# Optimization experiments

Measured on AMD Instinct MI355X. Metric: run time of the kernel, lower is better.

Reference implementation:

```python
import jax, jax.numpy as jnp
import numpy as np

B, L, D = 16, 1024, 256  # batch, c_len == q_len (required by the expand/add in the source), 2*d_model


def mask_logits(x, m):
    # Faithful to the source's (unusual) masking: x*m + x*(1-m)*1e30
    return x * m + x * (1.0 - m) * 1e30


def setup_inputs() -> dict:
    key = jax.random.key(0)
    k = jax.random.split(key, 7)
    c = jax.random.normal(k[0], (B, L, D), dtype=jnp.float32)
    q = jax.random.normal(k[1], (B, L, D), dtype=jnp.float32)
    c_mask = jnp.ones((B, 1, L), dtype=jnp.float32)
    q_mask = jnp.ones((B, 1, L), dtype=jnp.float32)
    # Learned parameters (nn.Parameter zeros in the source; random here so the test is non-degenerate)
    c_weight = jax.random.normal(k[2], (D, 1), dtype=jnp.float32) * 0.05
    q_weight = jax.random.normal(k[3], (D, 1), dtype=jnp.float32) * 0.05
    cq_weight = jax.random.normal(k[4], (1, 1, D), dtype=jnp.float32) * 0.05
    bias = jnp.zeros((1,), dtype=jnp.float32)
    return {"c": c, "q": q, "c_mask": c_mask, "q_mask": q_mask,
            "c_weight": c_weight, "q_weight": q_weight,
            "cq_weight": cq_weight, "bias": bias}


def reference(c, q, c_mask, q_mask, c_weight, q_weight, cq_weight, bias):
    # Dropout treated as identity (inference) for a deterministic reference.
    s0 = jnp.matmul(c, c_weight)                      # [B, L, 1] -> broadcasts over q_len
    s1 = jnp.swapaxes(jnp.matmul(c, q_weight), 1, 2)  # [B, 1, L] (source uses c here, not q)
    s2 = jnp.einsum('bid,bjd->bij', c * cq_weight, q) # [B, L, L]
    S = s0 + s1 + s2 + bias                           # trilinear similarity
    S1 = jax.nn.softmax(mask_logits(S, q_mask), axis=-1)              # [B, Lc, Lq]
    C2Q = jnp.matmul(S1, q)                                           # [B, Lc, D]
    # torch F.softmax with no dim on a 3D tensor defaults to dim=0 (legacy behavior) -> axis=0
    S2 = jax.nn.softmax(mask_logits(jnp.swapaxes(S, 1, 2), c_mask), axis=0)  # [B, Lq, Lc]
    S2 = jnp.matmul(S1, S2)                                           # [B, Lc, Lc]
    Q2C = jnp.matmul(S2, c)                                           # [B, Lc, D]
    # torch.cat default dim=0 -> [4B, Lc, D]
    return jnp.concatenate((c, C2Q, c * C2Q, c * Q2C), axis=0)
```

## Files before the change

### kernel.cpp

```cpp
#include <hip/hip_runtime.h>

typedef __bf16 bf16;
typedef _Float16 f16;
typedef __attribute__((ext_vector_type(8))) __bf16 bf16x8;
typedef __attribute__((ext_vector_type(4))) __bf16 bf16x4;
typedef __attribute__((ext_vector_type(8))) _Float16 f16x8;
typedef __attribute__((ext_vector_type(4))) _Float16 f16x4;
typedef __attribute__((ext_vector_type(4))) float f32x4;

constexpr int Bn = 16, Ln = 1024, Dn = 256;

__device__ __forceinline__ float maskf(float m) { return m + (1.0f - m) * 1e30f; }

__device__ __forceinline__ void gload16(const void* g, void* l) {
  __builtin_amdgcn_global_load_lds((const __attribute__((address_space(1))) void*)g,
                                   (__attribute__((address_space(3))) void*)l, 16, 0, 0);
}

__device__ __forceinline__ void stageA64(const bf16* __restrict__ A, int lda, int k0,
                                         bf16* lA, int tid, int wid) {
  int row = tid >> 2, kk = (tid & 3) << 3;
  gload16(A + (size_t)row * lda + k0 + kk, lA + (wid << 6) * 8);
}
__device__ __forceinline__ void stageB128(const bf16* __restrict__ B, int ldb, int k0,
                                          bf16* lB, int tid, int wid) {
#pragma unroll
  for (int p = 0; p < 2; ++p) {
    int c0 = tid + (p << 8);
    int row = c0 >> 2, kk = (c0 & 3) << 3;
    gload16(B + (size_t)row * ldb + k0 + kk, lB + ((p << 8) + (wid << 6)) * 8);
  }
}

__global__ __launch_bounds__(256) void k_prep2(
    const float* __restrict__ c, const float* __restrict__ q,
    const float* __restrict__ cw, const float* __restrict__ qw,
    const float* __restrict__ cqw, bf16* __restrict__ cm, bf16* __restrict__ qb,
    bf16* __restrict__ cT, bf16* __restrict__ qT,
    float* __restrict__ s0, float* __restrict__ s1, float* __restrict__ outc) {
  __shared__ __align__(16) bf16 tc[32][264];
  __shared__ __align__(16) bf16 tq[32][264];
  int blk = blockIdx.x;
  int b = blk >> 5;
  int l0 = (blk & 31) << 5;
  int t = threadIdx.x;
  int rl = t >> 3;
  int c0 = (t & 7) << 5;
  int grow = b * Ln + l0 + rl;
  size_t base = (size_t)grow * Dn + c0;
  float4 cv[8], qv[8];
#pragma unroll
  for (int k = 0; k < 8; ++k) {
    cv[k] = *(const float4*)&c[base + k * 4];
    qv[k] = *(const float4*)&q[base + k * 4];
  }
  float d0 = 0.f, d1 = 0.f;
#pragma unroll
  for (int k = 0; k < 8; ++k) {
    float4 w = *(const float4*)&cw[c0 + k * 4];
    float4 u = *(const float4*)&qw[c0 + k * 4];
    d0 += cv[k].x * w.x + cv[k].y * w.y + cv[k].z * w.z + cv[k].w * w.w;
    d1 += cv[k].x * u.x + cv[k].y * u.y + cv[k].z * u.z + cv[k].w * u.w;
  }
  d0 += __shfl_xor(d0, 1); d0 += __shfl_xor(d0, 2); d0 += __shfl_xor(d0, 4);
  d1 += __shfl_xor(d1, 1); d1 += __shfl_xor(d1, 2); d1 += __shfl_xor(d1, 4);
  if ((t & 7) == 0) { s0[grow] = d0; s1[grow] = d1; }
#pragma unroll
  for (int k = 0; k < 8; ++k) *(float4*)&outc[base + k * 4] = cv[k];
#pragma unroll
  for (int k2 = 0; k2 < 4; ++k2) {
    float4 m0 = *(const float4*)&cqw[c0 + k2 * 8];
    float4 m1 = *(const float4*)&cqw[c0 + k2 * 8 + 4];
    bf16x8 vm, vq, vc;
#pragma unroll
    for (int e = 0; e < 8; ++e) {
      float cvv = ((const float*)&cv[k2 * 2 + (e >> 2)])[e & 3];
      float qvv = ((const float*)&qv[k2 * 2 + (e >> 2)])[e & 3];
      float mw = (e < 4) ? ((const float*)&m0)[e] : ((const float*)&m1)[e - 4];
      vm[e] = (bf16)(cvv * mw);
      vq[e] = (bf16)qvv;
      vc[e] = (bf16)cvv;
    }
    *(bf16x8*)&cm[base + k2 * 8] = vm;
    *(bf16x8*)&qb[base + k2 * 8] = vq;
    *(bf16x8*)&tc[rl][c0 + k2 * 8] = vc;
    *(bf16x8*)&tq[rl][c0 + k2 * 8] = vq;
  }
  __syncthreads();
  int d = t;
  size_t tb = ((size_t)b * Dn + d) * Ln + l0;
  bf16x8 o[4];
#pragma unroll
  for (int j = 0; j < 4; ++j)
#pragma unroll
    for (int e = 0; e < 8; ++e) o[j][e] = tc[j * 8 + e][d];
#pragma unroll
  for (int j = 0; j < 4; ++j) *(bf16x8*)&cT[tb + j * 8] = o[j];
#pragma unroll
  for (int j = 0; j < 4; ++j)
#pragma unroll
    for (int e = 0; e < 8; ++e) o[j][e] = tq[j * 8 + e][d];
#pragma unroll
  for (int j = 0; j < 4; ++j) *(bf16x8*)&qT[tb + j * 8] = o[j];
}

__global__ __launch_bounds__(256) void g_s(const bf16* __restrict__ Am,
                                           const bf16* __restrict__ Bm,
                                           const float* __restrict__ s0,
                                           const float* __restrict__ s1,
                                           const float* __restrict__ bias,
                                           f16* __restrict__ S) {
  __shared__ __align__(16) bf16 lds[2][256 * 32];
  int f = blockIdx.x;
  int o = (f & 7) * 128 + (f >> 3);
  int bx = o & 7, by = (o >> 3) & 7, b = o >> 6;
  const bf16* Ab = Am + (size_t)b * Ln * Dn + (size_t)by * 128 * Dn;
  const bf16* Bb = Bm + (size_t)b * Ln * Dn + (size_t)bx * 128 * Dn;
  const int tid = threadIdx.x, wid = tid >> 6, lane = tid & 63;
  const int r = lane & 15, h = lane >> 4, wr = wid >> 1, wc = wid & 1;
  f32x4 acc[4][4];
  f32x4 zero = {0.f, 0.f, 0.f, 0.f};
#pragma unroll
  for (int i = 0; i < 4; ++i)
#pragma unroll
    for (int j = 0; j < 4; ++j) acc[i][j] = zero;

  stageB128(Ab, Dn, 0, &lds[0][0], tid, wid);
  stageB128(Bb, Dn, 0, &lds[0][128 * 32], tid, wid);
  __syncthreads();
  for (int t = 0; t < 8; ++t) {
    int cur = t & 1;
    if (t < 7) {
      stageB128(Ab, Dn, (t + 1) * 32, &lds[cur ^ 1][0], tid, wid);
      stageB128(Bb, Dn, (t + 1) * 32, &lds[cur ^ 1][128 * 32], tid, wid);
    }
    const bf16* lA = &lds[cur][0];
    const bf16* lB = &lds[cur][128 * 32];
    bf16x8 av[4], bv[4];
#pragma unroll
    for (int i = 0; i < 4; ++i) {
      av[i] = *(const bf16x8*)(lA + ((wr << 6) + (i << 4) + r) * 32 + (h << 3));
      bv[i] = *(const bf16x8*)(lB + ((wc << 6) + (i << 4) + r) * 32 + (h << 3));
    }
#pragma unroll
    for (int i = 0; i < 4; ++i)
#pragma unroll
      for (int j = 0; j < 4; ++j)
        acc[i][j] = __builtin_amdgcn_mfma_f32_16x16x32_bf16(av[i], bv[j], acc[i][j], 0, 0, 0);
    __syncthreads();
  }
  int grow = by * 128 + wr * 64, gcol = bx * 128 + wc * 64;
  float bvv = bias[0];
  size_t sb = (size_t)b * Ln * Ln;
#pragma unroll
  for (int j = 0; j < 4; ++j) {
    int n = gcol + j * 16 + r;
    float v1 = s1[b * Ln + n];
#pragma unroll
    for (int i = 0; i < 4; ++i) {
      int mb = grow + i * 16 + h * 4;
#pragma unroll
      for (int g = 0; g < 4; ++g) {
        float v0 = s0[b * Ln + mb + g];
        S[sb + (size_t)(mb + g) * Ln + n] = (f16)(acc[i][j][g] + v0 + v1 + bvv);
      }
    }
  }
}

__global__ __launch_bounds__(256) void k_rowsoftmax(const f16* __restrict__ S,
                                                    const float* __restrict__ qmask,
                                                    bf16* __restrict__ P1) {
  int t = threadIdx.x;
  int row = blockIdx.x * 4 + (t >> 6);
  int b = row >> 10;
  int lane = t & 63;
  const f16* Sr = S + (size_t)row * Ln;
  const float* qm = qmask + (size_t)b * Ln;
  float v[16];
  float mx = -3.4e38f;
#pragma unroll
  for (int p = 0; p < 2; ++p) {
    f16x8 x = ((const f16x8*)Sr)[lane + (p << 6)];
    float4 m0 = ((const float4*)qm)[(lane + (p << 6)) * 2];
    float4 m1 = ((const float4*)qm)[(lane + (p << 6)) * 2 + 1];
    float mm[8] = {m0.x, m0.y, m0.z, m0.w, m1.x, m1.y, m1.z, m1.w};
#pragma unroll
    for (int e = 0; e < 8; ++e) {
      float xv = (float)x[e] * maskf(mm[e]);
      v[8 * p + e] = xv;
      mx = fmaxf(mx, xv);
    }
  }
#pragma unroll
  for (int off = 32; off; off >>= 1) mx = fmaxf(mx, __shfl_xor(mx, off));
  float sum = 0.f;
#pragma unroll
  for (int k = 0; k < 16; ++k) {
    v[k] = __expf(v[k] - mx);
    sum += v[k];
  }
#pragma unroll
  for (int off = 32; off; off >>= 1) sum += __shfl_xor(sum, off);
  float inv = 1.0f / sum;
  bf16* Pr = P1 + (size_t)row * Ln;
#pragma unroll
  for (int p = 0; p < 2; ++p) {
    bf16x8 o;
#pragma unroll
    for (int e = 0; e < 8; ++e) o[e] = (bf16)(v[8 * p + e] * inv);
    ((bf16x8*)Pr)[lane + (p << 6)] = o;
  }
}

__global__ __launch_bounds__(256) void k_bp2(const f16* __restrict__ S,
                                             const float* __restrict__ cmask,
                                             bf16* __restrict__ P2) {
  __shared__ __align__(16) bf16 tile[16][32][36];
  int i0 = blockIdx.y * 32, j0 = blockIdx.x * 32;
  int t = threadIdx.x;
  int ti = t >> 3, tj4 = (t & 7) << 2;
  int i = i0 + ti;
  const f16* Sp = S + (size_t)i * Ln + j0 + tj4;
  float fm[16];
#pragma unroll
  for (int b = 0; b < 16; ++b) fm[b] = maskf(cmask[b * Ln + i]);
  float m[4] = {-3.4e38f, -3.4e38f, -3.4e38f, -3.4e38f};
#pragma unroll
  for (int b = 0; b < 16; ++b) {
    f16x4 u = *(const f16x4*)(Sp + (size_t)b * Ln * Ln);
#pragma unroll
    for (int g = 0; g < 4; ++g) m[g] = fmaxf(m[g], (float)u[g] * fm[b]);
  }
  float s[4] = {0.f, 0.f, 0.f, 0.f};
#pragma unroll
  for (int b = 0; b < 16; ++b) {
    f16x4 u = *(const f16x4*)(Sp + (size_t)b * Ln * Ln);
#pragma unroll
    for (int g = 0; g < 4; ++g) s[g] += __expf((float)u[g] * fm[b] - m[g]);
  }
#pragma unroll
  for (int g = 0; g < 4; ++g) s[g] = 1.0f / s[g];
#pragma unroll
  for (int b = 0; b < 16; ++b) {
    f16x4 u = *(const f16x4*)(Sp + (size_t)b * Ln * Ln);
#pragma unroll
    for (int g = 0; g < 4; ++g)
      tile[b][tj4 + g][ti] = (bf16)(__expf((float)u[g] * fm[b] - m[g]) * s[g]);
  }
  __syncthreads();
  int jl = t >> 3, i4 = (t & 7) << 2;
#pragma unroll
  for (int b = 0; b < 16; ++b) {
    *(bf16x4*)&P2[((size_t)b * Ln + j0 + jl) * Ln + i0 + i4] =
        *(const bf16x4*)&tile[b][jl][i4];
  }
}

__global__ __launch_bounds__(256) void g_t(const bf16* __restrict__ cT,
                                           const bf16* __restrict__ P2,
                                           bf16* __restrict__ TT) {
  __shared__ __align__(16) bf16 lds[2][192 * 32];
  int f = blockIdx.x;
  int o = (f & 7) * 64 + (f >> 3);
  int b = o >> 5, md = (o >> 3) & 3, nb = o & 7;
  const bf16* Ab = cT + (size_t)b * Dn * Ln + (size_t)md * 64 * Ln;
  const bf16* Bb = P2 + (size_t)b * Ln * Ln + (size_t)nb * 128 * Ln;
  const int tid = threadIdx.x, wid = tid >> 6, lane = tid & 63;
  const int r = lane & 15, h = lane >> 4, wr = wid >> 1, wc = wid & 1;
  f32x4 acc[2][4];
  f32x4 zero = {0.f, 0.f, 0.f, 0.f};
#pragma unroll
  for (int i = 0; i < 2; ++i)
#pragma unroll
    for (int j = 0; j < 4; ++j) acc[i][j] = zero;

  stageA64(Ab, Ln, 0, &lds[0][0], tid, wid);
  stageB128(Bb, Ln, 0, &lds[0][64 * 32], tid, wid);
  __syncthreads();
  for (int t = 0; t < 32; ++t) {
    int cur = t & 1;
    if (t < 31) {
      stageA64(Ab, Ln, (t + 1) * 32, &lds[cur ^ 1][0], tid, wid);
      stageB128(Bb, Ln, (t + 1) * 32, &lds[cur ^ 1][64 * 32], tid, wid);
    }
    const bf16* lA = &lds[cur][0];
    const bf16* lB = &lds[cur][64 * 32];
    bf16x8 av[2], bv[4];
#pragma unroll
    for (int i = 0; i < 2; ++i)
      av[i] = *(const bf16x8*)(lA + ((wr << 5) + (i << 4) + r) * 32 + (h << 3));
#pragma unroll
    for (int j = 0; j < 4; ++j)
      bv[j] = *(const bf16x8*)(lB + ((wc << 6) + (j << 4) + r) * 32 + (h << 3));
#pragma unroll
    for (int i = 0; i < 2; ++i)
#pragma unroll
      for (int j = 0; j < 4; ++j)
        acc[i][j] = __builtin_amdgcn_mfma_f32_16x16x32_bf16(av[i], bv[j], acc[i][j], 0, 0, 0);
    __syncthreads();
  }
  size_t ob = (size_t)b * Dn * Ln;
  int dbase = md * 64 + wr * 32, cbase = nb * 128 + wc * 64;
#pragma unroll
  for (int i = 0; i < 2; ++i)
#pragma unroll
    for (int j = 0; j < 4; ++j) {
      int n = cbase + j * 16 + r;
#pragma unroll
      for (int g = 0; g < 4; ++g)
        TT[ob + (size_t)(dbase + i * 16 + h * 4 + g) * Ln + n] = (bf16)acc[i][j][g];
    }
}

__global__ __launch_bounds__(256) void g_cq(const bf16* __restrict__ P1,
                                            const bf16* __restrict__ qT,
                                            const bf16* __restrict__ TT,
                                            const float* __restrict__ c,
                                            float* __restrict__ out) {
  __shared__ __align__(16) bf16 lds[2][192 * 32];
  int f = blockIdx.x;
  int o = (f & 7) * 128 + (f >> 3);
  int b = o >> 6, by = (o >> 2) & 15, bx = o & 3;
  const bf16* Ab = P1 + (size_t)b * Ln * Ln + (size_t)by * 64 * Ln;
  const bf16* B1 = qT + (size_t)b * Dn * Ln + (size_t)bx * 64 * Ln;
  const bf16* B2 = TT + (size_t)b * Dn * Ln + (size_t)bx * 64 * Ln;
  const int tid = threadIdx.x, wid = tid >> 6, lane = tid & 63;
  const int r = lane & 15, h = lane >> 4, wr = wid >> 1, wc = wid & 1;
  f32x4 acc1[2][2], acc2[2][2];
  f32x4 zero = {0.f, 0.f, 0.f, 0.f};
#pragma unroll
  for (int i = 0; i < 2; ++i)
#pragma unroll
    for (int j = 0; j < 2; ++j) { acc1[i][j] = zero; acc2[i][j] = zero; }

  stageA64(Ab, Ln, 0, &lds[0][0], tid, wid);
  stageA64(B1, Ln, 0, &lds[0][2048], tid, wid);
  stageA64(B2, Ln, 0, &lds[0][4096], tid, wid);
  __syncthreads();
  for (int t = 0; t < 32; ++t) {
    int cur = t & 1;
    if (t < 31) {
      stageA64(Ab, Ln, (t + 1) * 32, &lds[cur ^ 1][0], tid, wid);
      stageA64(B1, Ln, (t + 1) * 32, &lds[cur ^ 1][2048], tid, wid);
      stageA64(B2, Ln, (t + 1) * 32, &lds[cur ^ 1][4096], tid, wid);
    }
    const bf16* lA = &lds[cur][0];
    const bf16* lB1 = &lds[cur][2048];
    const bf16* lB2 = &lds[cur][4096];
    bf16x8 av[2], bv[2];
#pragma unroll
    for (int i = 0; i < 2; ++i)
      av[i] = *(const bf16x8*)(lA + ((wr << 5) + (i << 4) + r) * 32 + (h << 3));
#pragma unroll
    for (int j = 0; j < 2; ++j)
      bv[j] = *(const bf16x8*)(lB1 + ((wc << 5) + (j << 4) + r) * 32 + (h << 3));
#pragma unroll
    for (int i = 0; i < 2; ++i)
#pragma unroll
      for (int j = 0; j < 2; ++j)
        acc1[i][j] = __builtin_amdgcn_mfma_f32_16x16x32_bf16(av[i], bv[j], acc1[i][j], 0, 0, 0);
#pragma unroll
    for (int j = 0; j < 2; ++j)
      bv[j] = *(const bf16x8*)(lB2 + ((wc << 5) + (j << 4) + r) * 32 + (h << 3));
#pragma unroll
    for (int i = 0; i < 2; ++i)
#pragma unroll
      for (int j = 0; j < 2; ++j)
        acc2[i][j] = __builtin_amdgcn_mfma_f32_16x16x32_bf16(av[i], bv[j], acc2[i][j], 0, 0, 0);
    __syncthreads();
  }

  int grow = by * 64 + wr * 32, gcol = bx * 64 + wc * 32;
  const float* cb = c + (size_t)b * Ln * Dn;
  float* o1 = out + (size_t)(1 * Bn + b) * Ln * Dn;
  float* o2 = out + (size_t)(2 * Bn + b) * Ln * Dn;
  float* o3 = out + (size_t)(3 * Bn + b) * Ln * Dn;
#pragma unroll
  for (int j = 0; j < 2; ++j) {
    int n = gcol + j * 16 + r;
#pragma unroll
    for (int i = 0; i < 2; ++i) {
      int mb = grow + i * 16 + h * 4;
#pragma unroll
      for (int g = 0; g < 4; ++g) {
        float v1 = acc1[i][j][g];
        float v2 = acc2[i][j][g];
        size_t off = (size_t)(mb + g) * Dn + n;
        float cc = cb[off];
        o1[off] = v1;
        o2[off] = cc * v1;
        o3[off] = cc * v2;
      }
    }
  }
}

extern "C" void kernel_launch(void* const* d_in, const int* in_sizes, int n_in,
                              void* d_out, int out_size, void* d_ws, size_t ws_size,
                              hipStream_t stream) {
  const float* c = (const float*)d_in[0];
  const float* q = (const float*)d_in[1];
  const float* cmask = (const float*)d_in[2];
  const float* qmask = (const float*)d_in[3];
  const float* cw = (const float*)d_in[4];
  const float* qw = (const float*)d_in[5];
  const float* cqw = (const float*)d_in[6];
  const float* bias = (const float*)d_in[7];
  float* out = (float*)d_out;

  char* w = (char*)d_ws;
  f16* S = (f16*)w;       w += (size_t)Bn * Ln * Ln * 2;
  bf16* P1 = (bf16*)w;    w += (size_t)Bn * Ln * Ln * 2;
  bf16* P2 = (bf16*)w;    w += (size_t)Bn * Ln * Ln * 2;
  bf16* cm = (bf16*)w;    w += (size_t)Bn * Ln * Dn * 2;
  bf16* qb = (bf16*)w;    w += (size_t)Bn * Ln * Dn * 2;
  bf16* cT = (bf16*)w;    w += (size_t)Bn * Dn * Ln * 2;
  bf16* qT = (bf16*)w;    w += (size_t)Bn * Dn * Ln * 2;
  bf16* TT = (bf16*)w;    w += (size_t)Bn * Dn * Ln * 2;
  float* s0 = (float*)w;  w += (size_t)Bn * Ln * 4;
  float* s1 = (float*)w;  w += (size_t)Bn * Ln * 4;
  if ((size_t)(w - (char*)d_ws) > ws_size) return;

  k_prep2<<<dim3(Bn * Ln / 32), 256, 0, stream>>>(c, q, cw, qw, cqw, cm, qb, cT, qT, s0, s1, out);
  g_s<<<dim3(1024), 256, 0, stream>>>(cm, qb, s0, s1, bias, S);
  k_rowsoftmax<<<dim3(Bn * Ln / 4), 256, 0, stream>>>(S, qmask, P1);
  k_bp2<<<dim3(Ln / 32, Ln / 32), 256, 0, stream>>>(S, cmask, P2);
  g_t<<<dim3(512), 256, 0, stream>>>(cT, P2, TT);
  g_cq<<<dim3(1024), 256, 0, stream>>>(P1, qT, TT, c, out);
}
```

Before: 132.4 us.

## Double K-tile depth to 64 with XOR-swizzled LDS layout in g_t and g_cq

The two GEMM kernels g_t and g_cq now stage 64-wide K slices instead of 32. That halves the main-loop iterations and the block-wide barriers, and each stage holds two MFMA k-steps. The LDS tiles use a 64-element row stride with an XOR swizzle of the 16-byte slot by row, meant to avoid bank conflicts on the fragment reads. LDS use per block doubles, to 48KB in g_t, which may lower occupancy.

```diff
diff --git a/kernel.cpp b/kernel.cpp
--- a/kernel.cpp
+++ b/kernel.cpp
@@ -17,11 +17,6 @@
                                    (__attribute__((address_space(3))) void*)l, 16, 0, 0);
 }
 
-__device__ __forceinline__ void stageA64(const bf16* __restrict__ A, int lda, int k0,
-                                         bf16* lA, int tid, int wid) {
-  int row = tid >> 2, kk = (tid & 3) << 3;
-  gload16(A + (size_t)row * lda + k0 + kk, lA + (wid << 6) * 8);
-}
 __device__ __forceinline__ void stageB128(const bf16* __restrict__ B, int ldb, int k0,
                                           bf16* lB, int tid, int wid) {
 #pragma unroll
@@ -30,6 +25,31 @@
     int row = c0 >> 2, kk = (c0 & 3) << 3;
     gload16(B + (size_t)row * ldb + k0 + kk, lB + ((p << 8) + (wid << 6)) * 8);
   }
+}
+
+__device__ __forceinline__ void stageSwz64(const bf16* __restrict__ G, int ldg, int k0,
+                                           bf16* L, int tid, int wid) {
+#pragma unroll
+  for (int p = 0; p < 2; ++p) {
+    int u = tid + (p << 8);
+    int row = u >> 3, s = u & 7;
+    int kk = ((s ^ (row & 7)) << 3);
+    gload16(G + (size_t)row * ldg + k0 + kk, L + ((p << 8) + (wid << 6)) * 8);
+  }
+}
+__device__ __forceinline__ void stageSwz128(const bf16* __restrict__ G, int ldg, int k0,
+                                            bf16* L, int tid, int wid) {
+#pragma unroll
+  for (int p = 0; p < 4; ++p) {
+    int u = tid + (p << 8);
+    int row = u >> 3, s = u & 7;
+    int kk = ((s ^ (row & 7)) << 3);
+    gload16(G + (size_t)row * ldg + k0 + kk, L + ((p << 8) + (wid << 6)) * 8);
+  }
+}
+
+__device__ __forceinline__ const bf16* swzp(const bf16* L, int row, int slot) {
+  return L + row * 64 + ((slot ^ (row & 7)) << 3);
 }
 
 __global__ __launch_bounds__(256) void k_prep2(
@@ -260,7 +280,7 @@
 __global__ __launch_bounds__(256) void g_t(const bf16* __restrict__ cT,
                                            const bf16* __restrict__ P2,
                                            bf16* __restrict__ TT) {
-  __shared__ __align__(16) bf16 lds[2][192 * 32];
+  __shared__ __align__(16) bf16 lds[2][192 * 64];
   int f = blockIdx.x;
   int o = (f & 7) * 64 + (f >> 3);
   int b = o >> 5, md = (o >> 3) & 3, nb = o & 7;
@@ -275,29 +295,33 @@
 #pragma unroll
     for (int j = 0; j < 4; ++j) acc[i][j] = zero;
 
-  stageA64(Ab, Ln, 0, &lds[0][0], tid, wid);
-  stageB128(Bb, Ln, 0, &lds[0][64 * 32], tid, wid);
+  stageSwz64(Ab, Ln, 0, &lds[0][0], tid, wid);
+  stageSwz128(Bb, Ln, 0, &lds[0][64 * 64], tid, wid);
   __syncthreads();
-  for (int t = 0; t < 32; ++t) {
+  for (int t = 0; t < 16; ++t) {
     int cur = t & 1;
-    if (t < 31) {
-      stageA64(Ab, Ln, (t + 1) * 32, &lds[cur ^ 1][0], tid, wid);
-      stageB128(Bb, Ln, (t + 1) * 32, &lds[cur ^ 1][64 * 32], tid, wid);
+    if (t < 15) {
+      stageSwz64(Ab, Ln, (t + 1) * 64, &lds[cur ^ 1][0], tid, wid);
+      stageSwz128(Bb, Ln, (t + 1) * 64, &lds[cur ^ 1][64 * 64], tid, wid);
     }
     const bf16* lA = &lds[cur][0];
-    const bf16* lB = &lds[cur][64 * 32];
-    bf16x8 av[2], bv[4];
-#pragma unroll
-    for (int i = 0; i < 2; ++i)
-      av[i] = *(const bf16x8*)(lA + ((wr << 5) + (i << 4) + r) * 32 + (h << 3));
-#pragma unroll
-    for (int j = 0; j < 4; ++j)
-      bv[j] = *(const bf16x8*)(lB + ((wc << 6) + (j << 4) + r) * 32 + (h << 3));
-#pragma unroll
-    for (int i = 0; i < 2; ++i)
+    const bf16* lB = &lds[cur][64 * 64];
+#pragma unroll
+    for (int kk2 = 0; kk2 < 2; ++kk2) {
+      int slot = (kk2 << 2) | h;
+      bf16x8 av[2], bv[4];
+#pragma unroll
+      for (int i = 0; i < 2; ++i)
+        av[i] = *(const bf16x8*)swzp(lA, (wr << 5) + (i << 4) + r, slot);
 #pragma unroll
       for (int j = 0; j < 4; ++j)
-        acc[i][j] = __builtin_amdgcn_mfma_f32_16x16x32_bf16(av[i], bv[j], acc[i][j], 0, 0, 0);
+        bv[j] = *(const bf16x8*)swzp(lB, (wc << 6) + (j << 4) + r, slot);
+#pragma unroll
+      for (int i = 0; i < 2; ++i)
+#pragma unroll
+        for (int j = 0; j < 4; ++j)
+          acc[i][j] = __builtin_amdgcn_mfma_f32_16x16x32_bf16(av[i], bv[j], acc[i][j], 0, 0, 0);
+    }
     __syncthreads();
   }
   size_t ob = (size_t)b * Dn * Ln;
@@ -318,7 +342,7 @@
                                             const bf16* __restrict__ TT,
                                             const float* __restrict__ c,
                                             float* __restrict__ out) {
-  __shared__ __align__(16) bf16 lds[2][192 * 32];
+  __shared__ __align__(16) bf16 lds[2][192 * 64];
   int f = blockIdx.x;
   int o = (f & 7) * 128 + (f >> 3);
   int b = o >> 6, by = (o >> 2) & 15, bx = o & 3;
@@ -334,40 +358,44 @@
 #pragma unroll
     for (int j = 0; j < 2; ++j) { acc1[i][j] = zero; acc2[i][j] = zero; }
 
-  stageA64(Ab, Ln, 0, &lds[0][0], tid, wid);
-  stageA64(B1, Ln, 0, &lds[0][2048], tid, wid);
-  stageA64(B2, Ln, 0, &lds[0][4096], tid, wid);
+  stageSwz64(Ab, Ln, 0, &lds[0][0], tid, wid);
+  stageSwz64(B1, Ln, 0, &lds[0][4096], tid, wid);
+  stageSwz64(B2, Ln, 0, &lds[0][8192], tid, wid);
   __syncthreads();
-  for (int t = 0; t < 32; ++t) {
+  for (int t = 0; t < 16; ++t) {
     int cur = t & 1;
-    if (t < 31) {
-      stageA64(Ab, Ln, (t + 1) * 32, &lds[cur ^ 1][0], tid, wid);
-      stageA64(B1, Ln, (t + 1) * 32, &lds[cur ^ 1][2048], tid, wid);
-      stageA64(B2, Ln, (t + 1) * 32, &lds[cur ^ 1][4096], tid, wid);
+    if (t < 15) {
+      stageSwz64(Ab, Ln, (t + 1) * 64, &lds[cur ^ 1][0], tid, wid);
+      stageSwz64(B1, Ln, (t + 1) * 64, &lds[cur ^ 1][4096], tid, wid);
+      stageSwz64(B2, Ln, (t + 1) * 64, &lds[cur ^ 1][8192], tid, wid);
     }
     const bf16* lA = &lds[cur][0];
-    const bf16* lB1 = &lds[cur][2048];
-    const bf16* lB2 = &lds[cur][4096];
-    bf16x8 av[2], bv[2];
-#pragma unroll
-    for (int i = 0; i < 2; ++i)
-      av[i] = *(const bf16x8*)(lA + ((wr << 5) + (i << 4) + r) * 32 + (h << 3));
-#pragma unroll
-    for (int j = 0; j < 2; ++j)
-      bv[j] = *(const bf16x8*)(lB1 + ((wc << 5) + (j << 4) + r) * 32 + (h << 3));
-#pragma unroll
-    for (int i = 0; i < 2; ++i)
+    const bf16* lB1 = &lds[cur][4096];
+    const bf16* lB2 = &lds[cur][8192];
+#pragma unroll
+    for (int kk2 = 0; kk2 < 2; ++kk2) {
+      int slot = (kk2 << 2) | h;
+      bf16x8 av[2], bv[2];
+#pragma unroll
+      for (int i = 0; i < 2; ++i)
+        av[i] = *(const bf16x8*)swzp(lA, (wr << 5) + (i << 4) + r, slot);
 #pragma unroll
       for (int j = 0; j < 2; ++j)
-        acc1[i][j] = __builtin_amdgcn_mfma_f32_16x16x32_bf16(av[i], bv[j], acc1[i][j], 0, 0, 0);
-#pragma unroll
-    for (int j = 0; j < 2; ++j)
-      bv[j] = *(const bf16x8*)(lB2 + ((wc << 5) + (j << 4) + r) * 32 + (h << 3));
-#pragma unroll
-    for (int i = 0; i < 2; ++i)
+        bv[j] = *(const bf16x8*)swzp(lB1, (wc << 5) + (j << 4) + r, slot);
+#pragma unroll
+      for (int i = 0; i < 2; ++i)
+#pragma unroll
+        for (int j = 0; j < 2; ++j)
+          acc1[i][j] = __builtin_amdgcn_mfma_f32_16x16x32_bf16(av[i], bv[j], acc1[i][j], 0, 0, 0);
 #pragma unroll
       for (int j = 0; j < 2; ++j)
-        acc2[i][j] = __builtin_amdgcn_mfma_f32_16x16x32_bf16(av[i], bv[j], acc2[i][j], 0, 0, 0);
+        bv[j] = *(const bf16x8*)swzp(lB2, (wc << 5) + (j << 4) + r, slot);
+#pragma unroll
+      for (int i = 0; i < 2; ++i)
+#pragma unroll
+        for (int j = 0; j < 2; ++j)
+          acc2[i][j] = __builtin_amdgcn_mfma_f32_16x16x32_bf16(av[i], bv[j], acc2[i][j], 0, 0, 0);
+    }
     __syncthreads();
   }
 
```

After: 122.6 us. 1.08x faster.

## Enlarge GEMM tiles to 128x128, replace syncthreads with vmcnt waits, cache k_bp2 loads

Applied to the files above, without the earlier changes.

The g_t and g_cq GEMMs move from 64-wide to 128x128 output tiles, which halves or quarters the grid and increases operand reuse from LDS. All three GEMMs replace __syncthreads with explicit s_waitcnt vmcnt plus a raw barrier, so the next prefetch can stay in flight while the current stage is consumed. k_bp2 loads its 16 batch values once into registers and keeps the exponentials, instead of reloading S and recomputing exp three times. In exchange the larger tiles raise register and LDS use, and the grids shrink to 256 blocks, which may underfill the 256 CUs.

```diff
diff --git a/kernel.cpp b/kernel.cpp
--- a/kernel.cpp
+++ b/kernel.cpp
@@ -17,11 +17,15 @@
                                    (__attribute__((address_space(3))) void*)l, 16, 0, 0);
 }
 
-__device__ __forceinline__ void stageA64(const bf16* __restrict__ A, int lda, int k0,
-                                         bf16* lA, int tid, int wid) {
-  int row = tid >> 2, kk = (tid & 3) << 3;
-  gload16(A + (size_t)row * lda + k0 + kk, lA + (wid << 6) * 8);
-}
+#define VMCNT(N) asm volatile("s_waitcnt vmcnt(" #N ")" ::: "memory")
+#define LGKM0 asm volatile("s_waitcnt lgkmcnt(0)" ::: "memory")
+#define BARR                                  \
+  do {                                        \
+    asm volatile("" ::: "memory");            \
+    __builtin_amdgcn_s_barrier();             \
+    asm volatile("" ::: "memory");            \
+  } while (0)
+
 __device__ __forceinline__ void stageB128(const bf16* __restrict__ B, int ldb, int k0,
                                           bf16* lB, int tid, int wid) {
 #pragma unroll
@@ -127,13 +131,16 @@
 
   stageB128(Ab, Dn, 0, &lds[0][0], tid, wid);
   stageB128(Bb, Dn, 0, &lds[0][128 * 32], tid, wid);
-  __syncthreads();
   for (int t = 0; t < 8; ++t) {
     int cur = t & 1;
     if (t < 7) {
       stageB128(Ab, Dn, (t + 1) * 32, &lds[cur ^ 1][0], tid, wid);
       stageB128(Bb, Dn, (t + 1) * 32, &lds[cur ^ 1][128 * 32], tid, wid);
-    }
+      VMCNT(4);
+    } else {
+      VMCNT(0);
+    }
+    BARR;
     const bf16* lA = &lds[cur][0];
     const bf16* lB = &lds[cur][128 * 32];
     bf16x8 av[4], bv[4];
@@ -147,7 +154,7 @@
 #pragma unroll
       for (int j = 0; j < 4; ++j)
         acc[i][j] = __builtin_amdgcn_mfma_f32_16x16x32_bf16(av[i], bv[j], acc[i][j], 0, 0, 0);
-    __syncthreads();
+    LGKM0; BARR;
   }
   int grow = by * 128 + wr * 64, gcol = bx * 128 + wc * 64;
   float bvv = bias[0];
@@ -225,29 +232,29 @@
   float fm[16];
 #pragma unroll
   for (int b = 0; b < 16; ++b) fm[b] = maskf(cmask[b * Ln + i]);
+  f16x4 u[16];
+#pragma unroll
+  for (int b = 0; b < 16; ++b) u[b] = *(const f16x4*)(Sp + (size_t)b * Ln * Ln);
   float m[4] = {-3.4e38f, -3.4e38f, -3.4e38f, -3.4e38f};
 #pragma unroll
-  for (int b = 0; b < 16; ++b) {
-    f16x4 u = *(const f16x4*)(Sp + (size_t)b * Ln * Ln);
-#pragma unroll
-    for (int g = 0; g < 4; ++g) m[g] = fmaxf(m[g], (float)u[g] * fm[b]);
-  }
+  for (int b = 0; b < 16; ++b)
+#pragma unroll
+    for (int g = 0; g < 4; ++g) m[g] = fmaxf(m[g], (float)u[b][g] * fm[b]);
+  float e[16][4];
   float s[4] = {0.f, 0.f, 0.f, 0.f};
 #pragma unroll
-  for (int b = 0; b < 16; ++b) {
-    f16x4 u = *(const f16x4*)(Sp + (size_t)b * Ln * Ln);
-#pragma unroll
-    for (int g = 0; g < 4; ++g) s[g] += __expf((float)u[g] * fm[b] - m[g]);
-  }
+  for (int b = 0; b < 16; ++b)
+#pragma unroll
+    for (int g = 0; g < 4; ++g) {
+      e[b][g] = __expf((float)u[b][g] * fm[b] - m[g]);
+      s[g] += e[b][g];
+    }
 #pragma unroll
   for (int g = 0; g < 4; ++g) s[g] = 1.0f / s[g];
 #pragma unroll
-  for (int b = 0; b < 16; ++b) {
-    f16x4 u = *(const f16x4*)(Sp + (size_t)b * Ln * Ln);
-#pragma unroll
-    for (int g = 0; g < 4; ++g)
-      tile[b][tj4 + g][ti] = (bf16)(__expf((float)u[g] * fm[b] - m[g]) * s[g]);
-  }
+  for (int b = 0; b < 16; ++b)
+#pragma unroll
+    for (int g = 0; g < 4; ++g) tile[b][tj4 + g][ti] = (bf16)(e[b][g] * s[g]);
   __syncthreads();
   int jl = t >> 3, i4 = (t & 7) << 2;
 #pragma unroll
@@ -260,50 +267,52 @@
 __global__ __launch_bounds__(256) void g_t(const bf16* __restrict__ cT,
                                            const bf16* __restrict__ P2,
                                            bf16* __restrict__ TT) {
-  __shared__ __align__(16) bf16 lds[2][192 * 32];
+  __shared__ __align__(16) bf16 lds[2][256 * 32];
   int f = blockIdx.x;
-  int o = (f & 7) * 64 + (f >> 3);
-  int b = o >> 5, md = (o >> 3) & 3, nb = o & 7;
-  const bf16* Ab = cT + (size_t)b * Dn * Ln + (size_t)md * 64 * Ln;
+  int o = (f & 7) * 32 + (f >> 3);
+  int b = o >> 4, md = (o >> 3) & 1, nb = o & 7;
+  const bf16* Ab = cT + (size_t)b * Dn * Ln + (size_t)md * 128 * Ln;
   const bf16* Bb = P2 + (size_t)b * Ln * Ln + (size_t)nb * 128 * Ln;
   const int tid = threadIdx.x, wid = tid >> 6, lane = tid & 63;
   const int r = lane & 15, h = lane >> 4, wr = wid >> 1, wc = wid & 1;
-  f32x4 acc[2][4];
+  f32x4 acc[4][4];
   f32x4 zero = {0.f, 0.f, 0.f, 0.f};
 #pragma unroll
-  for (int i = 0; i < 2; ++i)
+  for (int i = 0; i < 4; ++i)
 #pragma unroll
     for (int j = 0; j < 4; ++j) acc[i][j] = zero;
 
-  stageA64(Ab, Ln, 0, &lds[0][0], tid, wid);
-  stageB128(Bb, Ln, 0, &lds[0][64 * 32], tid, wid);
-  __syncthreads();
+  stageB128(Ab, Ln, 0, &lds[0][0], tid, wid);
+  stageB128(Bb, Ln, 0, &lds[0][128 * 32], tid, wid);
   for (int t = 0; t < 32; ++t) {
     int cur = t & 1;
     if (t < 31) {
-      stageA64(Ab, Ln, (t + 1) * 32, &lds[cur ^ 1][0], tid, wid);
-      stageB128(Bb, Ln, (t + 1) * 32, &lds[cur ^ 1][64 * 32], tid, wid);
-    }
+      stageB128(Ab, Ln, (t + 1) * 32, &lds[cur ^ 1][0], tid, wid);
+      stageB128(Bb, Ln, (t + 1) * 32, &lds[cur ^ 1][128 * 32], tid, wid);
+      VMCNT(4);
+    } else {
+      VMCNT(0);
+    }
+    BARR;
     const bf16* lA = &lds[cur][0];
-    const bf16* lB = &lds[cur][64 * 32];
-    bf16x8 av[2], bv[4];
-#pragma unroll
-    for (int i = 0; i < 2; ++i)
-      av[i] = *(const bf16x8*)(lA + ((wr << 5) + (i << 4) + r) * 32 + (h << 3));
-#pragma unroll
-    for (int j = 0; j < 4; ++j)
-      bv[j] = *(const bf16x8*)(lB + ((wc << 6) + (j << 4) + r) * 32 + (h << 3));
-#pragma unroll
-    for (int i = 0; i < 2; ++i)
+    const bf16* lB = &lds[cur][128 * 32];
+    bf16x8 av[4], bv[4];
+#pragma unroll
+    for (int i = 0; i < 4; ++i) {
+      av[i] = *(const bf16x8*)(lA + ((wr << 6) + (i << 4) + r) * 32 + (h << 3));
+      bv[i] = *(const bf16x8*)(lB + ((wc << 6) + (i << 4) + r) * 32 + (h << 3));
+    }
+#pragma unroll
+    for (int i = 0; i < 4; ++i)
 #pragma unroll
       for (int j = 0; j < 4; ++j)
         acc[i][j] = __builtin_amdgcn_mfma_f32_16x16x32_bf16(av[i], bv[j], acc[i][j], 0, 0, 0);
-    __syncthreads();
+    LGKM0; BARR;
   }
   size_t ob = (size_t)b * Dn * Ln;
-  int dbase = md * 64 + wr * 32, cbase = nb * 128 + wc * 64;
-#pragma unroll
-  for (int i = 0; i < 2; ++i)
+  int dbase = md * 128 + wr * 64, cbase = nb * 128 + wc * 64;
+#pragma unroll
+  for (int i = 0; i < 4; ++i)
 #pragma unroll
     for (int j = 0; j < 4; ++j) {
       int n = cbase + j * 16 + r;
@@ -318,69 +327,72 @@
                                             const bf16* __restrict__ TT,
                                             const float* __restrict__ c,
                                             float* __restrict__ out) {
-  __shared__ __align__(16) bf16 lds[2][192 * 32];
+  __shared__ __align__(16) bf16 lds[2][384 * 32];
   int f = blockIdx.x;
-  int o = (f & 7) * 128 + (f >> 3);
-  int b = o >> 6, by = (o >> 2) & 15, bx = o & 3;
-  const bf16* Ab = P1 + (size_t)b * Ln * Ln + (size_t)by * 64 * Ln;
-  const bf16* B1 = qT + (size_t)b * Dn * Ln + (size_t)bx * 64 * Ln;
-  const bf16* B2 = TT + (size_t)b * Dn * Ln + (size_t)bx * 64 * Ln;
+  int o = (f & 7) * 32 + (f >> 3);
+  int b = o >> 4, by = (o >> 1) & 7, bx = o & 1;
+  const bf16* Ab = P1 + (size_t)b * Ln * Ln + (size_t)by * 128 * Ln;
+  const bf16* B1 = qT + (size_t)b * Dn * Ln + (size_t)bx * 128 * Ln;
+  const bf16* B2 = TT + (size_t)b * Dn * Ln + (size_t)bx * 128 * Ln;
   const int tid = threadIdx.x, wid = tid >> 6, lane = tid & 63;
   const int r = lane & 15, h = lane >> 4, wr = wid >> 1, wc = wid & 1;
-  f32x4 acc1[2][2], acc2[2][2];
+  f32x4 acc1[4][4], acc2[4][4];
   f32x4 zero = {0.f, 0.f, 0.f, 0.f};
 #pragma unroll
-  for (int i = 0; i < 2; ++i)
-#pragma unroll
-    for (int j = 0; j < 2; ++j) { acc1[i][j] = zero; acc2[i][j] = zero; }
-
-  stageA64(Ab, Ln, 0, &lds[0][0], tid, wid);
-  stageA64(B1, Ln, 0, &lds[0][2048], tid, wid);
-  stageA64(B2, Ln, 0, &lds[0][4096], tid, wid);
-  __syncthreads();
+  for (int i = 0; i < 4; ++i)
+#pragma unroll
+    for (int j = 0; j < 4; ++j) { acc1[i][j] = zero; acc2[i][j] = zero; }
+
+  stageB128(Ab, Ln, 0, &lds[0][0], tid, wid);
+  stageB128(B1, Ln, 0, &lds[0][4096], tid, wid);
+  stageB128(B2, Ln, 0, &lds[0][8192], tid, wid);
   for (int t = 0; t < 32; ++t) {
     int cur = t & 1;
     if (t < 31) {
-      stageA64(Ab, Ln, (t + 1) * 32, &lds[cur ^ 1][0], tid, wid);
-      stageA64(B1, Ln, (t + 1) * 32, &lds[cur ^ 1][2048], tid, wid);
-      stageA64(B2, Ln, (t + 1) * 32, &lds[cur ^ 1][4096], tid, wid);
-    }
+      stageB128(Ab, Ln, (t + 1) * 32, &lds[cur ^ 1][0], tid, wid);
+      stageB128(B1, Ln, (t + 1) * 32, &lds[cur ^ 1][4096], tid, wid);
+      stageB128(B2, Ln, (t + 1) * 32, &lds[cur ^ 1][8192], tid, wid);
+      VMCNT(6);
+    } else {
+      VMCNT(0);
+    }
+    BARR;
     const bf16* lA = &lds[cur][0];
-    const bf16* lB1 = &lds[cur][2048];
-    const bf16* lB2 = &lds[cur][4096];
-    bf16x8 av[2], bv[2];
-#pragma unroll
-    for (int i = 0; i < 2; ++i)
-      av[i] = *(const bf16x8*)(lA + ((wr << 5) + (i << 4) + r) * 32 + (h << 3));
-#pragma unroll
-    for (int j = 0; j < 2; ++j)
-      bv[j] = *(const bf16x8*)(lB1 + ((wc << 5) + (j << 4) + r) * 32 + (h << 3));
-#pragma unroll
-    for (int i = 0; i < 2; ++i)
-#pragma unroll
-      for (int j = 0; j < 2; ++j)
+    const bf16* lB1 = &lds[cur][4096];
+    const bf16* lB2 = &lds[cur][8192];
+    bf16x8 av[4], bv[4];
+#pragma unroll
+    for (int i = 0; i < 4; ++i)
+      av[i] = *(const bf16x8*)(lA + ((wr << 6) + (i << 4) + r) * 32 + (h << 3));
+#pragma unroll
+    for (int j = 0; j < 4; ++j)
+      bv[j] = *(const bf16x8*)(lB1 + ((wc << 6) + (j << 4) + r) * 32 + (h << 3));
+#pragma unroll
+    for (int i = 0; i < 4; ++i)
+#pragma unroll
+      for (int j = 0; j < 4; ++j)
         acc1[i][j] = __builtin_amdgcn_mfma_f32_16x16x32_bf16(av[i], bv[j], acc1[i][j], 0, 0, 0);
 #pragma unroll
-    for (int j = 0; j < 2; ++j)
-      bv[j] = *(const bf16x8*)(lB2 + ((wc << 5) + (j << 4) + r) * 32 + (h << 3));
-#pragma unroll
-    for (int i = 0; i < 2; ++i)
-#pragma unroll
-      for (int j = 0; j < 2; ++j)
+    for (int j = 0; j < 4; ++j)
+      bv[j] = *(const bf16x8*)(lB2 + ((wc << 6) + (j << 4) + r) * 32 + (h << 3));
+#pragma unroll
+    for (int i = 0; i < 4; ++i)
+#pragma unroll
+      for (int j = 0; j < 4; ++j)
         acc2[i][j] = __builtin_amdgcn_mfma_f32_16x16x32_bf16(av[i], bv[j], acc2[i][j], 0, 0, 0);
-    __syncthreads();
-  }
-
-  int grow = by * 64 + wr * 32, gcol = bx * 64 + wc * 32;
+    LGKM0; BARR;
+  }
+
+  int grow = by * 128 + wr * 64, gcol = bx * 128 + wc * 64;
   const float* cb = c + (size_t)b * Ln * Dn;
   float* o1 = out + (size_t)(1 * Bn + b) * Ln * Dn;
   float* o2 = out + (size_t)(2 * Bn + b) * Ln * Dn;
   float* o3 = out + (size_t)(3 * Bn + b) * Ln * Dn;
 #pragma unroll
-  for (int j = 0; j < 2; ++j) {
+  for (int j = 0; j < 4; ++j) {
     int n = gcol + j * 16 + r;
 #pragma unroll
-    for (int i = 0; i < 2; ++i) {
+    for (int i = 0; i < 4; ++i) {
       int mb = grow + i * 16 + h * 4;
 #pragma unroll
       for (int g = 0; g < 4; ++g) {
@@ -426,6 +438,6 @@
   g_s<<<dim3(1024), 256, 0, stream>>>(cm, qb, s0, s1, bias, S);
   k_rowsoftmax<<<dim3(Bn * Ln / 4), 256, 0, stream>>>(S, qmask, P1);
   k_bp2<<<dim3(Ln / 32, Ln / 32), 256, 0, stream>>>(S, cmask, P2);
-  g_t<<<dim3(512), 256, 0, stream>>>(cT, P2, TT);
-  g_cq<<<dim3(1024), 256, 0, stream>>>(P1, qT, TT, c, out);
-}
+  g_t<<<dim3(256), 256, 0, stream>>>(cT, P2, TT);
+  g_cq<<<dim3(256), 256, 0, stream>>>(P1, qT, TT, c, out);
+}
```

Result: no change. 134.1 us (+1.3%).
